# Performance work log

Hardware: AMD Instinct MI355X
Metric: run time of the kernel (lower is better)

The kernel has to match this reference:

```python
import jax, jax.numpy as jnp
import numpy as np

N = 20000       # nodes
E = 640000      # random edges (self-loops appended -> E + N total)
G = 64          # graphs in batch
F_IN = 114
H1 = 3          # heads in layer 1
D2 = 128        # output_dim of layer 2
NEG = 0.2       # GATConv leaky_relu negative slope


def setup_inputs() -> dict:
    key = jax.random.key(0)
    ks = jax.random.split(key, 20)
    x = jax.random.normal(ks[0], (N, F_IN), jnp.float32)
    src = jax.random.randint(ks[1], (E,), 0, N, jnp.int32)
    dst = jax.random.randint(ks[2], (E,), 0, N, jnp.int32)
    loop = jnp.arange(N, dtype=jnp.int32)  # PyG add_self_loops=True
    edge_index = jnp.stack([jnp.concatenate([src, loop]),
                            jnp.concatenate([dst, loop])])
    batch = (jnp.arange(N) * G // N).astype(jnp.int32)  # every graph non-empty

    def lin(k, i, o):
        return jax.random.normal(k, (i, o), jnp.float32) * (1.0 / np.sqrt(i))

    return {
        "x": x, "edge_index": edge_index, "batch": batch,
        # GATConv 1: 114 -> 114 per head, 3 heads, concat
        "W1": lin(ks[3], F_IN, H1 * F_IN),
        "a_src1": jax.random.normal(ks[4], (H1, F_IN), jnp.float32) * 0.1,
        "a_dst1": jax.random.normal(ks[5], (H1, F_IN), jnp.float32) * 0.1,
        "b1": jnp.zeros((H1 * F_IN,), jnp.float32),
        # GATConv 2: 342 -> 128, 1 head
        "W2": lin(ks[6], H1 * F_IN, D2),
        "a_src2": jax.random.normal(ks[7], (1, D2), jnp.float32) * 0.1,
        "a_dst2": jax.random.normal(ks[8], (1, D2), jnp.float32) * 0.1,
        "b2": jnp.zeros((D2,), jnp.float32),
        # MLP head
        "Wg": lin(ks[9], D2, 64),  "bg": jnp.zeros((64,), jnp.float32),
        "Wf1": lin(ks[10], 64, 32), "bf1": jnp.zeros((32,), jnp.float32),
        "Wf2": lin(ks[11], 32, 16), "bf2": jnp.zeros((16,), jnp.float32),
        "Wo": lin(ks[12], 16, 1),   "bo": jnp.zeros((1,), jnp.float32),
    }


def gat_conv(x, edge_index, W, a_src, a_dst, b, heads, dim):
    """PyG GATConv (self-loops already in edge_index, eval mode)."""
    n = x.shape[0]
    h = (x @ W).reshape(n, heads, dim)             # [N,H,D]
    src, dst = edge_index[0], edge_index[1]
    alpha_s = jnp.sum(h * a_src, axis=-1)          # [N,H]
    alpha_d = jnp.sum(h * a_dst, axis=-1)          # [N,H]
    e = jax.nn.leaky_relu(alpha_s[src] + alpha_d[dst], NEG)  # [E,H]
    # segment softmax over destination nodes
    m = jax.ops.segment_max(e, dst, num_segments=n)
    ex = jnp.exp(e - m[dst])
    s = jax.ops.segment_sum(ex, dst, num_segments=n)
    alpha = ex / s[dst]                            # [E,H]
    out = jax.ops.segment_sum(h[src] * alpha[..., None], dst, num_segments=n)
    return out.reshape(n, heads * dim) + b


def reference(x, edge_index, batch, W1, a_src1, a_dst1, b1,
              W2, a_src2, a_dst2, b2, Wg, bg, Wf1, bf1, Wf2, bf2, Wo, bo):
    h = jax.nn.elu(gat_conv(x, edge_index, W1, a_src1, a_dst1, b1, H1, F_IN))
    h = jax.nn.relu(gat_conv(h, edge_index, W2, a_src2, a_dst2, b2, 1, D2))
    g = jax.ops.segment_max(h, batch, num_segments=G)   # global max pool [G,128]
    g = jax.nn.relu(g @ Wg + bg)
    g = jax.nn.relu(g @ Wf1 + bf1)
    g = jax.nn.relu(g @ Wf2 + bf2)
    return g @ Wo + bo                                  # [G,1]
```

## Files before the change

kernel.cpp:

```cpp
#include <hip/hip_runtime.h>

#define NN 20000
#define EE 660000
#define GG 64
#define FIN 114
#define H1 3
#define F1 342
#define D2 128
#define NEG 0.2f

typedef __attribute__((ext_vector_type(8))) short short8v;
typedef __attribute__((ext_vector_type(4))) float f32x4;
typedef unsigned short ushort_t;

__device__ inline unsigned fenc(float f) {
    unsigned u = __float_as_uint(f);
    return (u & 0x80000000u) ? ~u : (u | 0x80000000u);
}
__device__ inline float fdec(unsigned u) {
    return (u & 0x80000000u) ? __uint_as_float(u & 0x7FFFFFFFu) : __uint_as_float(~u);
}
__device__ inline float lrelu(float x) { return x > 0.f ? x : NEG * x; }

__device__ inline void split2(float x, ushort_t& hi, ushort_t& lo) {
    unsigned u = __float_as_uint(x);
    unsigned uh = u & 0xFFFF0000u;
    hi = (ushort_t)(uh >> 16);
    float r = x - __uint_as_float(uh);
    unsigned v = __float_as_uint(r);
    unsigned vh = (v + 0x7FFFu + ((v >> 16) & 1u)) & 0xFFFF0000u;
    lo = (ushort_t)(vh >> 16);
}

__global__ void k_wa(const float* __restrict__ W1, const float* __restrict__ aS,
                     const float* __restrict__ aD, float* __restrict__ was,
                     float* __restrict__ wad) {
    int tid = blockIdx.x * 256 + threadIdx.x;
    if (tid >= 2 * FIN * H1) return;
    int which = tid >= FIN * H1;
    int i = which ? tid - FIN * H1 : tid;
    int k = i / H1, h = i % H1;
    const float* a = which ? aD : aS;
    float s = 0.f;
    for (int d = 0; d < FIN; d++) s += W1[k * F1 + h * FIN + d] * a[h * FIN + d];
    (which ? wad : was)[i] = s;
}

__global__ void k_prep1m(const float* __restrict__ W1, ushort_t* __restrict__ W1Th,
                         ushort_t* __restrict__ W1Tl) {
    int tid = blockIdx.x * 256 + threadIdx.x;
    if (tid >= H1 * 128 * 128) return;
    int h = tid / (128 * 128);
    int rem = tid & (128 * 128 - 1);
    int c = rem >> 7, k = rem & 127;
    float v = (c < FIN && k < FIN) ? W1[k * F1 + h * FIN + c] : 0.f;
    ushort_t hi, lo;
    split2(v, hi, lo);
    W1Th[tid] = hi;
    W1Tl[tid] = lo;
}

__global__ void k_prep2m(const float* __restrict__ W2, ushort_t* __restrict__ W2Th,
                         ushort_t* __restrict__ W2Tl) {
    int tid = blockIdx.x * 256 + threadIdx.x;
    if (tid >= 128 * 384) return;
    int c = tid / 384;
    int hk = tid - c * 384;
    int h = hk >> 7, k = hk & 127;
    float v = (k < FIN) ? W2[(h * FIN + k) * D2 + c] : 0.f;
    ushort_t hi, lo;
    split2(v, hi, lo);
    W2Th[tid] = hi;
    W2Tl[tid] = lo;
}

__global__ __launch_bounds__(256) void k_alpha1x(const float* __restrict__ x,
                                                 const float* __restrict__ was,
                                                 const float* __restrict__ wad,
                                                 float* __restrict__ as1,
                                                 float* __restrict__ ad1) {
    int n = blockIdx.x * 4 + (threadIdx.x >> 6);
    int l = threadIdx.x & 63;
    if (n >= NN) return;
    float x0 = x[n * FIN + l];
    float x1 = (l < FIN - 64) ? x[n * FIN + 64 + l] : 0.f;
    float s[H1], d[H1];
#pragma unroll
    for (int h = 0; h < H1; h++) {
        float w0s = was[l * H1 + h], w0d = wad[l * H1 + h];
        float w1s = (l < FIN - 64) ? was[(64 + l) * H1 + h] : 0.f;
        float w1d = (l < FIN - 64) ? wad[(64 + l) * H1 + h] : 0.f;
        s[h] = x0 * w0s + x1 * w1s;
        d[h] = x0 * w0d + x1 * w1d;
    }
#pragma unroll
    for (int o = 32; o > 0; o >>= 1) {
#pragma unroll
        for (int h = 0; h < H1; h++) {
            s[h] += __shfl_down(s[h], o);
            d[h] += __shfl_down(d[h], o);
        }
    }
    if (l == 0) {
#pragma unroll
        for (int h = 0; h < H1; h++) {
            as1[n * H1 + h] = s[h];
            ad1[n * H1 + h] = d[h];
        }
    }
}

__global__ void k_count(const int* __restrict__ dst, int* __restrict__ cnt) {
    int e = blockIdx.x * 256 + threadIdx.x;
    if (e < EE) atomicAdd(&cnt[dst[e]], 1);
}

__global__ __launch_bounds__(1024) void k_scan(const int* __restrict__ cnt,
                                               int* __restrict__ off) {
    __shared__ int part[1024];
    int t = threadIdx.x;
    const int CH = 20;
    int loc[CH];
    int s = 0;
    int base = t * CH;
    for (int i = 0; i < CH; i++) {
        int idx = base + i;
        int v = (idx < NN) ? cnt[idx] : 0;
        loc[i] = s;
        s += v;
    }
    part[t] = s;
    __syncthreads();
    for (int d = 1; d < 1024; d <<= 1) {
        int v = (t >= d) ? part[t - d] : 0;
        __syncthreads();
        part[t] += v;
        __syncthreads();
    }
    int pre = (t == 0) ? 0 : part[t - 1];
    for (int i = 0; i < CH; i++) {
        int idx = base + i;
        if (idx < NN) off[idx] = pre + loc[i];
    }
    if (t == 1023) off[NN] = part[1023];
}

__global__ void k_scatter(const int* __restrict__ src, const int* __restrict__ dst,
                          const int* __restrict__ off, int* __restrict__ cur,
                          int* __restrict__ csr_src) {
    int e = blockIdx.x * 256 + threadIdx.x;
    if (e < EE) {
        int d = dst[e];
        int pos = off[d] + atomicAdd(&cur[d], 1);
        csr_src[pos] = src[e];
    }
}

__global__ __launch_bounds__(128) void k_aggx(const float* __restrict__ x,
                                              const float* __restrict__ as1,
                                              const float* __restrict__ ad1,
                                              const int* __restrict__ off,
                                              const int* __restrict__ csr_src,
                                              ushort_t* __restrict__ xgh,
                                              ushort_t* __restrict__ xgl) {
    int n = blockIdx.x, t = threadIdx.x;
    int e0 = off[n], e1 = off[n + 1];
    float adv0 = ad1[n * H1 + 0], adv1 = ad1[n * H1 + 1], adv2 = ad1[n * H1 + 2];
    __shared__ int ssrc[64];
    __shared__ float sw[64][H1];
    __shared__ float red[64][H1];
    float acc0 = 0.f, acc1 = 0.f, acc2 = 0.f;
    float ps0 = 0.f, ps1 = 0.f, ps2 = 0.f;
    for (int base = e0; base < e1; base += 64) {
        int c = min(64, e1 - base);
        __syncthreads();
        if (t < c) {
            int s = csr_src[base + t];
            ssrc[t] = s;
            float w0 = __expf(lrelu(as1[s * H1 + 0] + adv0));
            float w1 = __expf(lrelu(as1[s * H1 + 1] + adv1));
            float w2 = __expf(lrelu(as1[s * H1 + 2] + adv2));
            sw[t][0] = w0; sw[t][1] = w1; sw[t][2] = w2;
            ps0 += w0; ps1 += w1; ps2 += w2;
        }
        __syncthreads();
        if (t < FIN) {
            for (int j = 0; j < c; j++) {
                float xv = x[ssrc[j] * FIN + t];
                acc0 += xv * sw[j][0];
                acc1 += xv * sw[j][1];
                acc2 += xv * sw[j][2];
            }
        }
    }
    __syncthreads();
    if (t < 64) { red[t][0] = ps0; red[t][1] = ps1; red[t][2] = ps2; }
    __syncthreads();
    for (int sr = 32; sr > 0; sr >>= 1) {
        if (t < sr) {
            red[t][0] += red[t + sr][0];
            red[t][1] += red[t + sr][1];
            red[t][2] += red[t + sr][2];
        }
        __syncthreads();
    }
    float i0 = 1.f / red[0][0], i1 = 1.f / red[0][1], i2 = 1.f / red[0][2];
    float v0 = (t < FIN) ? acc0 * i0 : 0.f;
    float v1 = (t < FIN) ? acc1 * i1 : 0.f;
    float v2 = (t < FIN) ? acc2 * i2 : 0.f;
    ushort_t hi, lo;
    split2(v0, hi, lo);
    xgh[(size_t)0 * NN * 128 + n * 128 + t] = hi;
    xgl[(size_t)0 * NN * 128 + n * 128 + t] = lo;
    split2(v1, hi, lo);
    xgh[(size_t)1 * NN * 128 + n * 128 + t] = hi;
    xgl[(size_t)1 * NN * 128 + n * 128 + t] = lo;
    split2(v2, hi, lo);
    xgh[(size_t)2 * NN * 128 + n * 128 + t] = hi;
    xgl[(size_t)2 * NN * 128 + n * 128 + t] = lo;
}

__global__ __launch_bounds__(256) void k_gemm1m(const ushort_t* __restrict__ xgh,
                                                const ushort_t* __restrict__ xgl,
                                                const ushort_t* __restrict__ W1Th,
                                                const ushort_t* __restrict__ W1Tl,
                                                const float* __restrict__ b1,
                                                ushort_t* __restrict__ h1hi,
                                                ushort_t* __restrict__ h1lo) {
    int h = blockIdx.y;
    int rb = blockIdx.x * 128;
    int w = threadIdx.x >> 6, l = threadIdx.x & 63;
    int m = l & 15, g = l >> 4;
    int r0 = rb + w * 32 + m;
    int r1 = r0 + 16;
    bool ok0 = (r0 < NN), ok1 = (r1 < NN);
    const ushort_t* xh = xgh + (size_t)h * NN * 128;
    const ushort_t* xl = xgl + (size_t)h * NN * 128;
    const ushort_t* Bh = W1Th + (size_t)h * 128 * 128;
    const ushort_t* Bl = W1Tl + (size_t)h * 128 * 128;
    const short8v z8 = {0, 0, 0, 0, 0, 0, 0, 0};
    f32x4 acc0[8], acc1[8];
#pragma unroll
    for (int j = 0; j < 8; j++) {
        acc0[j] = (f32x4){0.f, 0.f, 0.f, 0.f};
        acc1[j] = (f32x4){0.f, 0.f, 0.f, 0.f};
    }
#pragma unroll
    for (int k0 = 0; k0 < 128; k0 += 32) {
        int ka = k0 + g * 8;
        short8v a0h = ok0 ? *(const short8v*)(xh + (size_t)r0 * 128 + ka) : z8;
        short8v a0l = ok0 ? *(const short8v*)(xl + (size_t)r0 * 128 + ka) : z8;
        short8v a1h = ok1 ? *(const short8v*)(xh + (size_t)r1 * 128 + ka) : z8;
        short8v a1l = ok1 ? *(const short8v*)(xl + (size_t)r1 * 128 + ka) : z8;
        short8v bh[8], bl[8];
#pragma unroll
        for (int j = 0; j < 8; j++) {
            size_t bo = (size_t)(j * 16 + m) * 128 + ka;
            bh[j] = *(const short8v*)(Bh + bo);
            bl[j] = *(const short8v*)(Bl + bo);
        }
#pragma unroll
        for (int j = 0; j < 8; j++) {
            acc0[j] = __builtin_amdgcn_mfma_f32_16x16x32_bf16(a0h, bh[j], acc0[j], 0, 0, 0);
            acc1[j] = __builtin_amdgcn_mfma_f32_16x16x32_bf16(a1h, bh[j], acc1[j], 0, 0, 0);
            acc0[j] = __builtin_amdgcn_mfma_f32_16x16x32_bf16(a0h, bl[j], acc0[j], 0, 0, 0);
            acc1[j] = __builtin_amdgcn_mfma_f32_16x16x32_bf16(a1h, bl[j], acc1[j], 0, 0, 0);
            acc0[j] = __builtin_amdgcn_mfma_f32_16x16x32_bf16(a0l, bh[j], acc0[j], 0, 0, 0);
            acc1[j] = __builtin_amdgcn_mfma_f32_16x16x32_bf16(a1l, bh[j], acc1[j], 0, 0, 0);
        }
    }
    ushort_t* Hh = h1hi + (size_t)h * NN * 128;
    ushort_t* Hl = h1lo + (size_t)h * NN * 128;
#pragma unroll
    for (int j = 0; j < 8; j++) {
        int c = j * 16 + m;
        float bv = (c < FIN) ? b1[h * FIN + c] : 0.f;
#pragma unroll
        for (int r = 0; r < 4; r++) {
            int orow0 = rb + w * 32 + g * 4 + r;
            int orow1 = orow0 + 16;
            if (orow0 < NN) {
                float v = acc0[j][r] + bv;
                v = v > 0.f ? v : expm1f(v);
                ushort_t hi = 0, lo = 0;
                if (c < FIN) split2(v, hi, lo);
                Hh[(size_t)orow0 * 128 + c] = hi;
                Hl[(size_t)orow0 * 128 + c] = lo;
            }
            if (orow1 < NN) {
                float v = acc1[j][r] + bv;
                v = v > 0.f ? v : expm1f(v);
                ushort_t hi = 0, lo = 0;
                if (c < FIN) split2(v, hi, lo);
                Hh[(size_t)orow1 * 128 + c] = hi;
                Hl[(size_t)orow1 * 128 + c] = lo;
            }
        }
    }
}

__global__ __launch_bounds__(256) void k_gemm2m(const ushort_t* __restrict__ h1hi,
                                                const ushort_t* __restrict__ h1lo,
                                                const ushort_t* __restrict__ W2Th,
                                                const ushort_t* __restrict__ W2Tl,
                                                float* __restrict__ h2) {
    int rb = blockIdx.x * 128;
    int w = threadIdx.x >> 6, l = threadIdx.x & 63;
    int m = l & 15, g = l >> 4;
    int r0 = rb + w * 32 + m;
    int r1 = r0 + 16;
    bool ok0 = (r0 < NN), ok1 = (r1 < NN);
    const short8v z8 = {0, 0, 0, 0, 0, 0, 0, 0};
    f32x4 acc0[8], acc1[8];
#pragma unroll
    for (int j = 0; j < 8; j++) {
        acc0[j] = (f32x4){0.f, 0.f, 0.f, 0.f};
        acc1[j] = (f32x4){0.f, 0.f, 0.f, 0.f};
    }
#pragma unroll
    for (int k0 = 0; k0 < 384; k0 += 32) {
        int hh = k0 >> 7;
        int kc = (k0 & 127) + g * 8;
        size_t a0o = ((size_t)hh * NN + (size_t)(ok0 ? r0 : 0)) * 128 + kc;
        size_t a1o = ((size_t)hh * NN + (size_t)(ok1 ? r1 : 0)) * 128 + kc;
        short8v a0h = ok0 ? *(const short8v*)(h1hi + a0o) : z8;
        short8v a0l = ok0 ? *(const short8v*)(h1lo + a0o) : z8;
        short8v a1h = ok1 ? *(const short8v*)(h1hi + a1o) : z8;
        short8v a1l = ok1 ? *(const short8v*)(h1lo + a1o) : z8;
        short8v bh[8], bl[8];
#pragma unroll
        for (int j = 0; j < 8; j++) {
            size_t bo = (size_t)(j * 16 + m) * 384 + k0 + g * 8;
            bh[j] = *(const short8v*)(W2Th + bo);
            bl[j] = *(const short8v*)(W2Tl + bo);
        }
#pragma unroll
        for (int j = 0; j < 8; j++) {
            acc0[j] = __builtin_amdgcn_mfma_f32_16x16x32_bf16(a0h, bh[j], acc0[j], 0, 0, 0);
            acc1[j] = __builtin_amdgcn_mfma_f32_16x16x32_bf16(a1h, bh[j], acc1[j], 0, 0, 0);
            acc0[j] = __builtin_amdgcn_mfma_f32_16x16x32_bf16(a0h, bl[j], acc0[j], 0, 0, 0);
            acc1[j] = __builtin_amdgcn_mfma_f32_16x16x32_bf16(a1h, bl[j], acc1[j], 0, 0, 0);
            acc0[j] = __builtin_amdgcn_mfma_f32_16x16x32_bf16(a0l, bh[j], acc0[j], 0, 0, 0);
            acc1[j] = __builtin_amdgcn_mfma_f32_16x16x32_bf16(a1l, bh[j], acc1[j], 0, 0, 0);
        }
    }
#pragma unroll
    for (int j = 0; j < 8; j++) {
        int c = j * 16 + m;
#pragma unroll
        for (int r = 0; r < 4; r++) {
            int orow0 = rb + w * 32 + g * 4 + r;
            int orow1 = orow0 + 16;
            if (orow0 < NN) h2[(size_t)orow0 * D2 + c] = acc0[j][r];
            if (orow1 < NN) h2[(size_t)orow1 * D2 + c] = acc1[j][r];
        }
    }
}

__global__ __launch_bounds__(256) void k_alpha2(const float* __restrict__ h2,
                                                const float* __restrict__ aS,
                                                const float* __restrict__ aD,
                                                float* __restrict__ as2,
                                                float* __restrict__ ad2) {
    int n = blockIdx.x * 4 + (threadIdx.x >> 6);
    int l = threadIdx.x & 63;
    if (n >= NN) return;
    float v0 = h2[(size_t)n * D2 + l], v1 = h2[(size_t)n * D2 + 64 + l];
    float ps = v0 * aS[l] + v1 * aS[64 + l];
    float pd = v0 * aD[l] + v1 * aD[64 + l];
    for (int o = 32; o > 0; o >>= 1) {
        ps += __shfl_down(ps, o);
        pd += __shfl_down(pd, o);
    }
    if (l == 0) {
        as2[n] = ps;
        ad2[n] = pd;
    }
}

__global__ __launch_bounds__(128) void k_agg2f(const float* __restrict__ h2,
                                               const float* __restrict__ as2,
                                               const float* __restrict__ ad2,
                                               const int* __restrict__ off,
                                               const int* __restrict__ csr_src,
                                               const float* __restrict__ b2,
                                               unsigned* __restrict__ poolbuf) {
    int n = blockIdx.x, t = threadIdx.x;
    int e0 = off[n], e1 = off[n + 1];
    float adv = ad2[n];
    __shared__ int ssrc[64];
    __shared__ float sw[64];
    __shared__ float red[64];
    float acc = 0.f, ps = 0.f;
    for (int base = e0; base < e1; base += 64) {
        int c = min(64, e1 - base);
        __syncthreads();
        if (t < c) {
            int s = csr_src[base + t];
            ssrc[t] = s;
            float w = __expf(lrelu(as2[s] + adv));
            sw[t] = w;
            ps += w;
        }
        __syncthreads();
        for (int j = 0; j < c; j++) acc += h2[(size_t)ssrc[j] * D2 + t] * sw[j];
    }
    __syncthreads();
    if (t < 64) red[t] = ps;
    __syncthreads();
    for (int sr = 32; sr > 0; sr >>= 1) {
        if (t < sr) red[t] += red[t + sr];
        __syncthreads();
    }
    float v = fmaxf(acc / red[0] + b2[t], 0.f);
    int g = (int)(((long long)n * GG) / NN);
    atomicMax(&poolbuf[g * D2 + t], fenc(v));
}

__global__ __launch_bounds__(128) void k_mlp(const unsigned* __restrict__ poolbuf,
                                             const float* __restrict__ Wg,
                                             const float* __restrict__ bg,
                                             const float* __restrict__ Wf1,
                                             const float* __restrict__ bf1,
                                             const float* __restrict__ Wf2,
                                             const float* __restrict__ bf2,
                                             const float* __restrict__ Wo,
                                             const float* __restrict__ bo,
                                             float* __restrict__ out) {
    int g = blockIdx.x;
    int t = threadIdx.x;
    __shared__ float pool[D2];
    __shared__ float a1[64];
    __shared__ float a2[32];
    __shared__ float a3[16];
    pool[t] = fdec(poolbuf[g * D2 + t]);
    __syncthreads();
    if (t < 64) {
        float acc = bg[t];
        for (int k = 0; k < D2; k++) acc += pool[k] * Wg[k * 64 + t];
        a1[t] = fmaxf(acc, 0.f);
    }
    __syncthreads();
    if (t < 32) {
        float acc = bf1[t];
        for (int k = 0; k < 64; k++) acc += a1[k] * Wf1[k * 32 + t];
        a2[t] = fmaxf(acc, 0.f);
    }
    __syncthreads();
    if (t < 16) {
        float acc = bf2[t];
        for (int k = 0; k < 32; k++) acc += a2[k] * Wf2[k * 16 + t];
        a3[t] = fmaxf(acc, 0.f);
    }
    __syncthreads();
    if (t == 0) {
        float acc = bo[0];
        for (int k = 0; k < 16; k++) acc += a3[k] * Wo[k];
        out[g] = acc;
    }
}

extern "C" void kernel_launch(void* const* d_in, const int* in_sizes, int n_in,
                              void* d_out, int out_size, void* d_ws, size_t ws_size,
                              hipStream_t stream) {
    const float* x = (const float*)d_in[0];
    const int* ei = (const int*)d_in[1];
    const float* W1 = (const float*)d_in[3];
    const float* aS1 = (const float*)d_in[4];
    const float* aD1 = (const float*)d_in[5];
    const float* b1 = (const float*)d_in[6];
    const float* W2 = (const float*)d_in[7];
    const float* aS2 = (const float*)d_in[8];
    const float* aD2 = (const float*)d_in[9];
    const float* b2 = (const float*)d_in[10];
    const float* Wg = (const float*)d_in[11];
    const float* bg = (const float*)d_in[12];
    const float* Wf1 = (const float*)d_in[13];
    const float* bf1 = (const float*)d_in[14];
    const float* Wf2 = (const float*)d_in[15];
    const float* bf2 = (const float*)d_in[16];
    const float* Wo = (const float*)d_in[17];
    const float* bo = (const float*)d_in[18];
    float* out = (float*)d_out;

    const int* src = ei;
    const int* dst = ei + EE;

    char* ws = (char*)d_ws;
    size_t o = 0;
    auto alloc = [&](size_t bytes) -> char* {
        char* p = ws + o;
        o += (bytes + 255) & ~(size_t)255;
        return p;
    };
    float* was = (float*)alloc((size_t)FIN * H1 * 4);
    float* wad = (float*)alloc((size_t)FIN * H1 * 4);
    ushort_t* W1Th = (ushort_t*)alloc((size_t)H1 * 128 * 128 * 2);
    ushort_t* W1Tl = (ushort_t*)alloc((size_t)H1 * 128 * 128 * 2);
    ushort_t* W2Th = (ushort_t*)alloc((size_t)128 * 384 * 2);
    ushort_t* W2Tl = (ushort_t*)alloc((size_t)128 * 384 * 2);
    float* as1 = (float*)alloc((size_t)NN * H1 * 4);
    float* ad1 = (float*)alloc((size_t)NN * H1 * 4);
    int* cnt = (int*)alloc((size_t)NN * 4);
    int* off = (int*)alloc((size_t)(NN + 1) * 4);
    int* cur = (int*)alloc((size_t)NN * 4);
    int* csr_src = (int*)alloc((size_t)EE * 4);
    ushort_t* xgh = (ushort_t*)alloc((size_t)H1 * NN * 128 * 2);
    ushort_t* xgl = (ushort_t*)alloc((size_t)H1 * NN * 128 * 2);
    ushort_t* h1hi = (ushort_t*)alloc((size_t)H1 * NN * 128 * 2);
    ushort_t* h1lo = (ushort_t*)alloc((size_t)H1 * NN * 128 * 2);
    float* h2 = (float*)alloc((size_t)NN * D2 * 4);
    float* as2 = (float*)alloc((size_t)NN * 4);
    float* ad2 = (float*)alloc((size_t)NN * 4);
    unsigned* poolbuf = (unsigned*)alloc((size_t)GG * D2 * 4);
    (void)ws_size;

    hipMemsetAsync(cnt, 0, (size_t)NN * 4, stream);
    hipMemsetAsync(cur, 0, (size_t)NN * 4, stream);
    hipMemsetAsync(poolbuf, 0, (size_t)GG * D2 * 4, stream);

    const int EB = (EE + 255) / 256;

    k_wa<<<(2 * FIN * H1 + 255) / 256, 256, 0, stream>>>(W1, aS1, aD1, was, wad);
    k_prep1m<<<(H1 * 128 * 128 + 255) / 256, 256, 0, stream>>>(W1, W1Th, W1Tl);
    k_prep2m<<<(128 * 384 + 255) / 256, 256, 0, stream>>>(W2, W2Th, W2Tl);
    k_alpha1x<<<(NN + 3) / 4, 256, 0, stream>>>(x, was, wad, as1, ad1);
    k_count<<<EB, 256, 0, stream>>>(dst, cnt);
    k_scan<<<1, 1024, 0, stream>>>(cnt, off);
    k_scatter<<<EB, 256, 0, stream>>>(src, dst, off, cur, csr_src);
    k_aggx<<<NN, 128, 0, stream>>>(x, as1, ad1, off, csr_src, xgh, xgl);
    k_gemm1m<<<dim3((NN + 127) / 128, H1), 256, 0, stream>>>(xgh, xgl, W1Th, W1Tl, b1, h1hi, h1lo);
    k_gemm2m<<<(NN + 127) / 128, 256, 0, stream>>>(h1hi, h1lo, W2Th, W2Tl, h2);
    k_alpha2<<<(NN + 3) / 4, 256, 0, stream>>>(h2, aS2, aD2, as2, ad2);
    k_agg2f<<<NN, 128, 0, stream>>>(h2, as2, ad2, off, csr_src, b2, poolbuf);
    k_mlp<<<GG, 128, 0, stream>>>(poolbuf, Wg, bg, Wf1, bf1, Wf2, bf2, Wo, bo, out);
}
```

Baseline: 300.7 us.

## Split edge aggregation into weight pass and column-chunked multi-slot gather kernels

Each fused per-node aggregation kernel is split in two. A 64-thread kernel computes the softmax edge weights and the inverse sums, and writes them to global buffers. A gather kernel then runs a 2D grid (node × 32-column chunk), where four slots each walk a strided subset of edges and combine their partial sums through a shuffle and shared memory. x is also padded to 128 columns beforehand so row reads are aligned. The aim is more parallelism per node and better latency hiding on the irregular gathers, at the cost of extra global traffic for the edge-weight buffers and the padded copy, plus more kernel launches.

```diff
diff --git a/kernel.cpp b/kernel.cpp
--- a/kernel.cpp
+++ b/kernel.cpp
@@ -72,6 +72,13 @@
     split2(v, hi, lo);
     W2Th[tid] = hi;
     W2Tl[tid] = lo;
+}
+
+__global__ void k_xp(const float* __restrict__ x, float* __restrict__ xP) {
+    int tid = blockIdx.x * 256 + threadIdx.x;
+    if (tid >= NN * 128) return;
+    int n = tid >> 7, c = tid & 127;
+    xP[tid] = (c < FIN) ? x[n * FIN + c] : 0.f;
 }
 
 __global__ __launch_bounds__(256) void k_alpha1x(const float* __restrict__ x,
@@ -156,68 +163,125 @@
     }
 }
 
-__global__ __launch_bounds__(128) void k_aggx(const float* __restrict__ x,
-                                              const float* __restrict__ as1,
-                                              const float* __restrict__ ad1,
-                                              const int* __restrict__ off,
-                                              const int* __restrict__ csr_src,
-                                              ushort_t* __restrict__ xgh,
-                                              ushort_t* __restrict__ xgl) {
+__global__ __launch_bounds__(64) void k_ew1(const float* __restrict__ as1,
+                                            const float* __restrict__ ad1,
+                                            const int* __restrict__ off,
+                                            const int* __restrict__ csr_src,
+                                            float* __restrict__ ew1,
+                                            float* __restrict__ sinv1) {
     int n = blockIdx.x, t = threadIdx.x;
     int e0 = off[n], e1 = off[n + 1];
     float adv0 = ad1[n * H1 + 0], adv1 = ad1[n * H1 + 1], adv2 = ad1[n * H1 + 2];
-    __shared__ int ssrc[64];
-    __shared__ float sw[64][H1];
-    __shared__ float red[64][H1];
-    float acc0 = 0.f, acc1 = 0.f, acc2 = 0.f;
-    float ps0 = 0.f, ps1 = 0.f, ps2 = 0.f;
-    for (int base = e0; base < e1; base += 64) {
-        int c = min(64, e1 - base);
-        __syncthreads();
-        if (t < c) {
-            int s = csr_src[base + t];
-            ssrc[t] = s;
-            float w0 = __expf(lrelu(as1[s * H1 + 0] + adv0));
-            float w1 = __expf(lrelu(as1[s * H1 + 1] + adv1));
-            float w2 = __expf(lrelu(as1[s * H1 + 2] + adv2));
-            sw[t][0] = w0; sw[t][1] = w1; sw[t][2] = w2;
-            ps0 += w0; ps1 += w1; ps2 += w2;
-        }
-        __syncthreads();
-        if (t < FIN) {
-            for (int j = 0; j < c; j++) {
-                float xv = x[ssrc[j] * FIN + t];
-                acc0 += xv * sw[j][0];
-                acc1 += xv * sw[j][1];
-                acc2 += xv * sw[j][2];
-            }
-        }
-    }
-    __syncthreads();
-    if (t < 64) { red[t][0] = ps0; red[t][1] = ps1; red[t][2] = ps2; }
-    __syncthreads();
-    for (int sr = 32; sr > 0; sr >>= 1) {
-        if (t < sr) {
-            red[t][0] += red[t + sr][0];
-            red[t][1] += red[t + sr][1];
-            red[t][2] += red[t + sr][2];
-        }
-        __syncthreads();
-    }
-    float i0 = 1.f / red[0][0], i1 = 1.f / red[0][1], i2 = 1.f / red[0][2];
-    float v0 = (t < FIN) ? acc0 * i0 : 0.f;
-    float v1 = (t < FIN) ? acc1 * i1 : 0.f;
-    float v2 = (t < FIN) ? acc2 * i2 : 0.f;
-    ushort_t hi, lo;
-    split2(v0, hi, lo);
-    xgh[(size_t)0 * NN * 128 + n * 128 + t] = hi;
-    xgl[(size_t)0 * NN * 128 + n * 128 + t] = lo;
-    split2(v1, hi, lo);
-    xgh[(size_t)1 * NN * 128 + n * 128 + t] = hi;
-    xgl[(size_t)1 * NN * 128 + n * 128 + t] = lo;
-    split2(v2, hi, lo);
-    xgh[(size_t)2 * NN * 128 + n * 128 + t] = hi;
-    xgl[(size_t)2 * NN * 128 + n * 128 + t] = lo;
+    float s0 = 0.f, s1 = 0.f, s2 = 0.f;
+    for (int e = e0 + t; e < e1; e += 64) {
+        int s = csr_src[e];
+        float w0 = __expf(lrelu(as1[s * H1 + 0] + adv0));
+        float w1 = __expf(lrelu(as1[s * H1 + 1] + adv1));
+        float w2 = __expf(lrelu(as1[s * H1 + 2] + adv2));
+        ew1[(size_t)0 * EE + e] = w0;
+        ew1[(size_t)1 * EE + e] = w1;
+        ew1[(size_t)2 * EE + e] = w2;
+        s0 += w0; s1 += w1; s2 += w2;
+    }
+#pragma unroll
+    for (int o = 32; o > 0; o >>= 1) {
+        s0 += __shfl_down(s0, o);
+        s1 += __shfl_down(s1, o);
+        s2 += __shfl_down(s2, o);
+    }
+    if (t == 0) {
+        sinv1[n * H1 + 0] = 1.f / s0;
+        sinv1[n * H1 + 1] = 1.f / s1;
+        sinv1[n * H1 + 2] = 1.f / s2;
+    }
+}
+
+__global__ __launch_bounds__(64) void k_ew2(const float* __restrict__ as2,
+                                            const float* __restrict__ ad2,
+                                            const int* __restrict__ off,
+                                            const int* __restrict__ csr_src,
+                                            float* __restrict__ ew2,
+                                            float* __restrict__ sinv2) {
+    int n = blockIdx.x, t = threadIdx.x;
+    int e0 = off[n], e1 = off[n + 1];
+    float adv = ad2[n];
+    float s = 0.f;
+    for (int e = e0 + t; e < e1; e += 64) {
+        float w = __expf(lrelu(as2[csr_src[e]] + adv));
+        ew2[e] = w;
+        s += w;
+    }
+#pragma unroll
+    for (int o = 32; o > 0; o >>= 1) s += __shfl_down(s, o);
+    if (t == 0) sinv2[n] = 1.f / s;
+}
+
+__global__ __launch_bounds__(128) void k_gx(const float* __restrict__ xP,
+                                            const float* __restrict__ ew1,
+                                            const float* __restrict__ sinv1,
+                                            const int* __restrict__ off,
+                                            const int* __restrict__ csr_src,
+                                            ushort_t* __restrict__ xgh,
+                                            ushort_t* __restrict__ xgl) {
+    int n = blockIdx.x, chunk = blockIdx.y;
+    int t = threadIdx.x;
+    int col = chunk * 32 + (t & 31);
+    int slot = t >> 5;
+    int e0 = off[n], e1 = off[n + 1];
+    float a0 = 0.f, a1 = 0.f, a2 = 0.f;
+    for (int e = e0 + slot; e < e1; e += 4) {
+        int s = csr_src[e];
+        float xv = xP[(size_t)s * 128 + col];
+        a0 += ew1[(size_t)0 * EE + e] * xv;
+        a1 += ew1[(size_t)1 * EE + e] * xv;
+        a2 += ew1[(size_t)2 * EE + e] * xv;
+    }
+    a0 += __shfl_xor(a0, 32);
+    a1 += __shfl_xor(a1, 32);
+    a2 += __shfl_xor(a2, 32);
+    __shared__ float red[32][H1];
+    if (t >= 64 && t < 96) {
+        red[t - 64][0] = a0; red[t - 64][1] = a1; red[t - 64][2] = a2;
+    }
+    __syncthreads();
+    if (t < 32) {
+        a0 += red[t][0]; a1 += red[t][1]; a2 += red[t][2];
+        float i0 = sinv1[n * H1 + 0], i1 = sinv1[n * H1 + 1], i2 = sinv1[n * H1 + 2];
+        ushort_t hi, lo;
+        size_t o0 = (size_t)0 * NN * 128 + (size_t)n * 128 + col;
+        size_t o1 = (size_t)1 * NN * 128 + (size_t)n * 128 + col;
+        size_t o2 = (size_t)2 * NN * 128 + (size_t)n * 128 + col;
+        split2(a0 * i0, hi, lo); xgh[o0] = hi; xgl[o0] = lo;
+        split2(a1 * i1, hi, lo); xgh[o1] = hi; xgl[o1] = lo;
+        split2(a2 * i2, hi, lo); xgh[o2] = hi; xgl[o2] = lo;
+    }
+}
+
+__global__ __launch_bounds__(128) void k_g2(const float* __restrict__ h2,
+                                            const float* __restrict__ ew2,
+                                            const float* __restrict__ sinv2,
+                                            const int* __restrict__ off,
+                                            const int* __restrict__ csr_src,
+                                            const float* __restrict__ b2,
+                                            unsigned* __restrict__ poolbuf) {
+    int n = blockIdx.x, chunk = blockIdx.y;
+    int t = threadIdx.x;
+    int col = chunk * 32 + (t & 31);
+    int slot = t >> 5;
+    int e0 = off[n], e1 = off[n + 1];
+    float acc = 0.f;
+    for (int e = e0 + slot; e < e1; e += 4)
+        acc += ew2[e] * h2[(size_t)csr_src[e] * 128 + col];
+    acc += __shfl_xor(acc, 32);
+    __shared__ float red[32];
+    if (t >= 64 && t < 96) red[t - 64] = acc;
+    __syncthreads();
+    if (t < 32) {
+        acc += red[t];
+        float v = fmaxf(acc * sinv2[n] + b2[col], 0.f);
+        int g = (int)(((long long)n * GG) / NN);
+        atomicMax(&poolbuf[g * D2 + col], fenc(v));
+    }
 }
 
 __global__ __launch_bounds__(256) void k_gemm1m(const ushort_t* __restrict__ xgh,
@@ -376,45 +440,6 @@
         as2[n] = ps;
         ad2[n] = pd;
     }
-}
-
-__global__ __launch_bounds__(128) void k_agg2f(const float* __restrict__ h2,
-                                               const float* __restrict__ as2,
-                                               const float* __restrict__ ad2,
-                                               const int* __restrict__ off,
-                                               const int* __restrict__ csr_src,
-                                               const float* __restrict__ b2,
-                                               unsigned* __restrict__ poolbuf) {
-    int n = blockIdx.x, t = threadIdx.x;
-    int e0 = off[n], e1 = off[n + 1];
-    float adv = ad2[n];
-    __shared__ int ssrc[64];
-    __shared__ float sw[64];
-    __shared__ float red[64];
-    float acc = 0.f, ps = 0.f;
-    for (int base = e0; base < e1; base += 64) {
-        int c = min(64, e1 - base);
-        __syncthreads();
-        if (t < c) {
-            int s = csr_src[base + t];
-            ssrc[t] = s;
-            float w = __expf(lrelu(as2[s] + adv));
-            sw[t] = w;
-            ps += w;
-        }
-        __syncthreads();
-        for (int j = 0; j < c; j++) acc += h2[(size_t)ssrc[j] * D2 + t] * sw[j];
-    }
-    __syncthreads();
-    if (t < 64) red[t] = ps;
-    __syncthreads();
-    for (int sr = 32; sr > 0; sr >>= 1) {
-        if (t < sr) red[t] += red[t + sr];
-        __syncthreads();
-    }
-    float v = fmaxf(acc / red[0] + b2[t], 0.f);
-    int g = (int)(((long long)n * GG) / NN);
-    atomicMax(&poolbuf[g * D2 + t], fenc(v));
 }
 
 __global__ __launch_bounds__(128) void k_mlp(const unsigned* __restrict__ poolbuf,
@@ -499,12 +524,17 @@
     ushort_t* W1Tl = (ushort_t*)alloc((size_t)H1 * 128 * 128 * 2);
     ushort_t* W2Th = (ushort_t*)alloc((size_t)128 * 384 * 2);
     ushort_t* W2Tl = (ushort_t*)alloc((size_t)128 * 384 * 2);
+    float* xP = (float*)alloc((size_t)NN * 128 * 4);
     float* as1 = (float*)alloc((size_t)NN * H1 * 4);
     float* ad1 = (float*)alloc((size_t)NN * H1 * 4);
     int* cnt = (int*)alloc((size_t)NN * 4);
     int* off = (int*)alloc((size_t)(NN + 1) * 4);
     int* cur = (int*)alloc((size_t)NN * 4);
     int* csr_src = (int*)alloc((size_t)EE * 4);
+    float* ew1 = (float*)alloc((size_t)H1 * EE * 4);
+    float* sinv1 = (float*)alloc((size_t)NN * H1 * 4);
+    float* ew2 = (float*)alloc((size_t)EE * 4);
+    float* sinv2 = (float*)alloc((size_t)NN * 4);
     ushort_t* xgh = (ushort_t*)alloc((size_t)H1 * NN * 128 * 2);
     ushort_t* xgl = (ushort_t*)alloc((size_t)H1 * NN * 128 * 2);
     ushort_t* h1hi = (ushort_t*)alloc((size_t)H1 * NN * 128 * 2);
@@ -524,14 +554,17 @@
     k_wa<<<(2 * FIN * H1 + 255) / 256, 256, 0, stream>>>(W1, aS1, aD1, was, wad);
     k_prep1m<<<(H1 * 128 * 128 + 255) / 256, 256, 0, stream>>>(W1, W1Th, W1Tl);
     k_prep2m<<<(128 * 384 + 255) / 256, 256, 0, stream>>>(W2, W2Th, W2Tl);
+    k_xp<<<(NN * 128 + 255) / 256, 256, 0, stream>>>(x, xP);
     k_alpha1x<<<(NN + 3) / 4, 256, 0, stream>>>(x, was, wad, as1, ad1);
     k_count<<<EB, 256, 0, stream>>>(dst, cnt);
     k_scan<<<1, 1024, 0, stream>>>(cnt, off);
     k_scatter<<<EB, 256, 0, stream>>>(src, dst, off, cur, csr_src);
-    k_aggx<<<NN, 128, 0, stream>>>(x, as1, ad1, off, csr_src, xgh, xgl);
+    k_ew1<<<NN, 64, 0, stream>>>(as1, ad1, off, csr_src, ew1, sinv1);
+    k_gx<<<dim3(NN, 4), 128, 0, stream>>>(xP, ew1, sinv1, off, csr_src, xgh, xgl);
     k_gemm1m<<<dim3((NN + 127) / 128, H1), 256, 0, stream>>>(xgh, xgl, W1Th, W1Tl, b1, h1hi, h1lo);
     k_gemm2m<<<(NN + 127) / 128, 256, 0, stream>>>(h1hi, h1lo, W2Th, W2Tl, h2);
     k_alpha2<<<(NN + 3) / 4, 256, 0, stream>>>(h2, aS2, aD2, as2, ad2);
-    k_agg2f<<<NN, 128, 0, stream>>>(h2, as2, ad2, off, csr_src, b2, poolbuf);
+    k_ew2<<<NN, 64, 0, stream>>>(as2, ad2, off, csr_src, ew2, sinv2);
+    k_g2<<<dim3(NN, 4), 128, 0, stream>>>(h2, ew2, sinv2, off, csr_src, b2, poolbuf);
     k_mlp<<<GG, 128, 0, stream>>>(poolbuf, Wg, bg, Wf1, bf1, Wf2, bf2, Wo, bo, out);
 }
```

Result: slower. 452.4 us (+50.5%).
